# Performance work log

Hardware: AMD Instinct MI355X
Metric: run time of the kernel (lower is better)

## Reference

```python
import jax, jax.numpy as jnp
import numpy as np

DEPTH = 3

def _rx(theta):
    c, s = jnp.cos(theta / 2), jnp.sin(theta / 2)
    return jnp.stack([jnp.stack([c + 0j, -1j * s], -1),
                      jnp.stack([-1j * s, c + 0j], -1)], -2)

def _ry(theta):
    c, s = jnp.cos(theta / 2), jnp.sin(theta / 2)
    return jnp.stack([jnp.stack([c + 0j, -s + 0j], -1),
                      jnp.stack([s + 0j, c + 0j], -1)], -2)

def _rz(theta):
    e = jnp.exp(-0.5j * theta.astype(jnp.complex64))
    z = jnp.zeros_like(e)
    return jnp.stack([jnp.stack([e, z], -1),
                      jnp.stack([z, jnp.conj(e)], -1)], -2)

def _apply_1q(state, U, q):
    # state: (batch, 2,2,...,2); wire q lives on axis q+1. U: (2,2) or (batch,2,2)
    s = jnp.moveaxis(state, q + 1, -1)
    if U.ndim == 3:
        s = jnp.einsum('b...i,bji->b...j', s, U)
    else:
        s = jnp.einsum('...i,ji->...j', s, U)
    return jnp.moveaxis(s, -1, q + 1)

def _apply_cnot(state, c, t):
    s = jnp.moveaxis(state, (c + 1, t + 1), (-2, -1))
    s = jnp.concatenate([s[..., 0:1, :], s[..., 1:2, ::-1]], axis=-2)
    return jnp.moveaxis(s, (-2, -1), (c + 1, t + 1))

def _circuit(x, params):
    batch, n = x.shape
    depth = params.shape[0]
    state = jnp.zeros((batch,) + (2,) * n, jnp.complex64)
    state = state.at[(slice(None),) + (0,) * n].set(1.0)
    # data-encoding RX with per-sample angles
    for q in range(n):
        state = _apply_1q(state, _rx(x[:, q].astype(jnp.complex64).real), q)
    for l in range(depth):
        for q in range(n):
            state = _apply_1q(state, _rx(params[l, q, 0]), q)
            state = _apply_1q(state, _ry(params[l, q, 1]), q)
            state = _apply_1q(state, _rz(params[l, q, 2]), q)
        for q in range(n - 1):
            state = _apply_cnot(state, q, q + 1)
        state = _apply_cnot(state, n - 1, 0)
    probs = state.real ** 2 + state.imag ** 2  # (batch, 2,...,2)
    exps = []
    for w in range(n):
        p = jnp.moveaxis(probs, w + 1, 1).reshape(batch, 2, -1).sum(-1)
        exps.append(p[:, 0] - p[:, 1])  # <Z_w> = P(0) - P(1)
    return jnp.stack(exps, axis=1)


def setup_inputs() -> dict:
    key = jax.random.key(0)
    k1, k2 = jax.random.split(key)
    batch, n = 128, 14
    x = jax.random.normal(k1, (batch, n), dtype=jnp.float32)
    params = jax.random.normal(k2, (DEPTH, n, 3), dtype=jnp.float32)
    return {"x": x, "params": params}


def reference(x, params):
    return _circuit(x, params)
```

## Files before the change

### kernel.cpp

```cpp
#include <hip/hip_runtime.h>

namespace {

using v2f = __attribute__((ext_vector_type(2))) float;

constexpr int NQ      = 14;
constexpr int NSTATES = 1 << NQ;
constexpr int BLOCK   = 1024;
constexpr int NWAVES  = BLOCK / 64;

constexpr unsigned cparity(unsigned x){ x^=x>>8; x^=x>>4; x^=x>>2; x^=x>>1; return x&1u; }

struct Mat { unsigned row[NQ]; unsigned col[NQ]; };

constexpr Mat m_after(int nr){
  Mat m{};
  for(int p=0;p<NQ;++p){ m.row[p]=1u<<p; m.col[p]=1u<<p; }
  for(int l=0;l<nr;++l)
    for(int q=0;q<NQ;++q){
      int cq=(q==NQ-1)?NQ-1:q, tq=(q==NQ-1)?0:q+1;
      int Pc=NQ-1-cq, Pt=NQ-1-tq;
      m.row[Pt]^=m.row[Pc]; m.col[Pc]^=m.col[Pt];
    }
  return m;
}

constexpr Mat M1=m_after(1), M2=m_after(2), M3=m_after(3);
constexpr unsigned amask(int q){ return M1.col[NQ-1-q]; }
constexpr unsigned arow (int q){ return M1.row[NQ-1-q]; }
constexpr unsigned bmask(int q){ return M2.col[NQ-1-q]; }
constexpr unsigned brow (int q){ return M2.row[NQ-1-q]; }

constexpr int rank_of(const unsigned* v, int n){
  unsigned a[24]{};
  for(int i=0;i<n;++i) a[i]=v[i];
  int r=0;
  for(int bit=15;bit>=0;--bit){
    int p=-1;
    for(int i=r;i<n;++i){ if((a[i]>>bit)&1){ p=i; break; } }
    if(p<0) continue;
    unsigned t=a[r]; a[r]=a[p]; a[p]=t;
    for(int i=0;i<n;++i) if(i!=r && ((a[i]>>bit)&1)) a[i]^=a[r];
    ++r;
  }
  return r;
}

struct Plan {
  unsigned A[14], B[14], C[14];
  int BlaneGi[6]; unsigned BlanePi4[6];
  int BregGi[4];  unsigned BregEps[4];
  int CregGi[4];  unsigned CregEps[4];
  int ClaneGi[4]; unsigned ClaneEps[4];
  unsigned EJ4[14], ET[14];
};

constexpr Plan make_plan(){
  Plan P{};
  for(int t=0;t<14;++t) P.A[t]=amask(t);
  for(int t=0;t<4;++t){ P.B[t]=amask(10+t); P.BregGi[t]=10+t; }
  bool used[14]{}; int picked[14]{}; int np=0;
  {
    unsigned cur[20]{}; int nc=0;
    for(int t=0;t<4;++t) cur[nc++]=P.B[t];
    for(int q=0;q<14 && np<10;++q){
      cur[nc]=bmask(q);
      if(rank_of(cur,nc+1)==nc+1){ ++nc; picked[np++]=q; used[q]=true; }
    }
  }
  for(int i=0;i<6;++i){ P.B[4+i]=bmask(picked[i]); P.BlaneGi[i]=14+picked[i]; }
  int wq[4]{}, un[4]{}; int nu=0;
  for(int i=0;i<4;++i){ wq[i]=picked[6+i]; P.B[10+i]=bmask(wq[i]); P.CregGi[i]=14+wq[i]; }
  for(int q=0;q<14;++q) if(!used[q]) un[nu++]=q;
  for(int i=0;i<4;++i) P.ClaneGi[i]=14+un[i];
  for(int i=0;i<4;++i){ unsigned m=0;
    for(int t=0;t<10;++t) m |= cparity(arow(10+i)&P.B[4+t])<<t;
    P.BregEps[i]=m; }
  for(int i=0;i<6;++i){ unsigned m=0;
    for(int t=0;t<4;++t) m |= cparity(brow(picked[i])&P.B[t])<<t;
    P.BlanePi4[i]=m; }
  for(int t=0;t<4;++t) P.C[t]=bmask(wq[t]);
  for(int t=0;t<4;++t) P.C[4+t]=bmask(un[t]);
  {
    unsigned cc[20]{}; int n=0;
    for(int t=0;t<8;++t) cc[n++]=P.C[t];
    int pos=8;
    for(int p=0;p<14 && pos<14;++p){
      cc[n]=1u<<p;
      if(rank_of(cc,n+1)==n+1){ P.C[pos]=1u<<p; ++n; ++pos; }
    }
  }
  for(int i=0;i<4;++i){ unsigned m=0;
    for(int t=0;t<10;++t) m |= cparity(brow(wq[i])&P.C[4+t])<<t;
    P.CregEps[i]=m; }
  for(int i=0;i<4;++i){ unsigned m=0;
    for(int t=0;t<10;++t){ if(t==i) continue; m |= cparity(brow(un[i])&P.C[4+t])<<t; }
    P.ClaneEps[i]=m; }
  for(int w=0;w<14;++w){
    unsigned R=M3.row[NQ-1-w]; unsigned mj=0, mt=0;
    for(int t=0;t<4;++t)  mj |= cparity(R&P.C[t])<<t;
    for(int t=0;t<10;++t) mt |= cparity(R&P.C[4+t])<<t;
    P.EJ4[w]=mj; P.ET[w]=mt;
  }
  return P;
}

constexpr Plan PL = make_plan();
static_assert(rank_of(PL.A,14)==14, "phase A map not bijective");
static_assert(rank_of(PL.B,14)==14, "phase B map not bijective");
static_assert(rank_of(PL.C,14)==14, "phase C map not bijective");

struct Inv { unsigned col[NQ]; };
constexpr Inv inv_basis(const unsigned* bas){
  unsigned vec[NQ]{}, cmb[NQ]{}; bool used[NQ]{}; int pivk[NQ]{};
  for(int k=0;k<NQ;++k){ vec[k]=bas[k]; cmb[k]=1u<<k; }
  for(int b=0;b<NQ;++b){
    int p=-1;
    for(int k=0;k<NQ;++k) if(!used[k] && ((vec[k]>>b)&1)){ p=k; break; }
    used[p]=true; pivk[b]=p;
    for(int k=0;k<NQ;++k) if(k!=p && ((vec[k]>>b)&1)){ vec[k]^=vec[p]; cmb[k]^=cmb[p]; }
  }
  Inv R{};
  for(int b=0;b<NQ;++b) R.col[b]=cmb[pivk[b]];
  return R;
}
constexpr bool check_inv(const unsigned* bas, const Inv& iv){
  for(int p=0;p<NQ;++p){
    unsigned s=0;
    for(int k=0;k<NQ;++k) if((iv.col[p]>>k)&1) s^=bas[k];
    if(s != (1u<<p)) return false;
  }
  return true;
}
constexpr Inv IA = inv_basis(PL.A), IB = inv_basis(PL.B), IC = inv_basis(PL.C);
static_assert(check_inv(PL.A, IA), "IA");
static_assert(check_inv(PL.B, IB), "IB");
static_assert(check_inv(PL.C, IC), "IC");

struct Trans { unsigned t[NQ]; };
constexpr Trans trans_phys(const Inv& iv){
  Trans T{};
  for(int p=0;p<NQ;++p) T.t[p]=iv.col[p];
  return T;
}
constexpr Trans trans_of(const unsigned* cur, const Inv& iv){
  Trans T{};
  for(int k=0;k<NQ;++k){
    unsigned c=0;
    for(int p=0;p<NQ;++p) if((cur[k]>>p)&1) c^=iv.col[p];
    T.t[k]=c;
  }
  return T;
}
constexpr Trans T_PA = trans_phys(IA);
constexpr Trans T_AB = trans_of(PL.A, IB);
constexpr Trans T_BC = trans_of(PL.B, IC);

struct CJ { unsigned v[16]; };
constexpr CJ mk_cj(const Trans& T){
  CJ c{};
  for(int j=0;j<16;++j){
    unsigned s=0;
    for(int b=0;b<4;++b) if((j>>b)&1) s^=T.t[b];
    c.v[j]=s;
  }
  return c;
}
constexpr CJ CJ_PA=mk_cj(T_PA), CJ_AB=mk_cj(T_AB), CJ_BC=mk_cj(T_BC);

__device__ __forceinline__ v2f mkv(float a, float b){ v2f r; r[0]=a; r[1]=b; return r; }

__device__ __forceinline__ v2f pk_mul(v2f a, v2f b){
  v2f d; asm("v_pk_mul_f32 %0, %1, %2 op_sel:[0,0] op_sel_hi:[1,1]" : "=v"(d) : "v"(a), "v"(b)); return d;
}
__device__ __forceinline__ v2f pk_fma(v2f a, v2f b, v2f c){
  v2f d; asm("v_pk_fma_f32 %0, %1, %2, %3 op_sel:[0,0,0] op_sel_hi:[1,1,1]" : "=v"(d) : "v"(a), "v"(b), "v"(c)); return d;
}
__device__ __forceinline__ v2f pk_fma_swap1(v2f a, v2f b, v2f c){
  v2f d; asm("v_pk_fma_f32 %0, %1, %2, %3 op_sel:[0,1,0] op_sel_hi:[1,0,1]" : "=v"(d) : "v"(a), "v"(b), "v"(c)); return d;
}
__device__ __forceinline__ v2f cmul_pk(v2f uxx, v2f uyn, v2f s){ return pk_fma_swap1(uyn, s, pk_mul(uxx, s)); }
__device__ __forceinline__ v2f cfma_pk(v2f uxx, v2f uyn, v2f s, v2f acc){ return pk_fma_swap1(uyn, s, pk_fma(uxx, s, acc)); }

__device__ __forceinline__ float2 cmulf(float2 a, float2 b){
  return make_float2(a.x*b.x - a.y*b.y, a.x*b.y + a.y*b.x);
}
__device__ __forceinline__ v2f sel2(bool c, v2f x, v2f y){ v2f r; r[0]=c?x[0]:y[0]; r[1]=c?x[1]:y[1]; return r; }

struct GC { v2f u00x,u00n,u01x,u01n,u10x,u10n,u11x,u11n; };
__device__ __forceinline__ GC load_gc(const v2f* __restrict__ g){
  GC c{g[0],g[1],g[2],g[3],g[4],g[5],g[6],g[7]}; return c;
}

template<int CTRL>
__device__ __forceinline__ int dpp(int x){
  return __builtin_amdgcn_update_dpp(0, x, CTRL, 0xF, 0xF, true);
}
__device__ __forceinline__ int x32(int x, unsigned lane){
  auto r = __builtin_amdgcn_permlane32_swap((unsigned)x, (unsigned)x, false, false);
  return (lane & 32u) ? (int)r[0] : (int)r[1];
}
template<int K>
__device__ __forceinline__ v2f xpart(v2f v, unsigned lane){
  int x0=__float_as_int(v[0]), x1=__float_as_int(v[1]);
  int y0, y1;
  if constexpr (K==0){ y0=dpp<0xB1>(x0);  y1=dpp<0xB1>(x1); }
  else if constexpr (K==1){ y0=dpp<0x4E>(x0);  y1=dpp<0x4E>(x1); }
  else if constexpr (K==2){
    y0=__builtin_amdgcn_ds_swizzle(x0,0x101F);
    y1=__builtin_amdgcn_ds_swizzle(x1,0x101F);
  }
  else if constexpr (K==3){ y0=dpp<0x128>(x0); y1=dpp<0x128>(x1); }
  else if constexpr (K==4){
    y0=__builtin_amdgcn_ds_swizzle(x0,0x401F);
    y1=__builtin_amdgcn_ds_swizzle(x1,0x401F);
  }
  else { y0=x32(x0,lane); y1=x32(x1,lane); }
  v2f r; r[0]=__int_as_float(y0); r[1]=__int_as_float(y1); return r;
}

template<int BIT>
__device__ __forceinline__ void reg_gate(v2f (&a)[16], const GC& c, bool eps){
  v2f m00x=sel2(eps,c.u11x,c.u00x), m00n=sel2(eps,c.u11n,c.u00n);
  v2f m01x=sel2(eps,c.u10x,c.u01x), m01n=sel2(eps,c.u10n,c.u01n);
  v2f m10x=sel2(eps,c.u01x,c.u10x), m10n=sel2(eps,c.u01n,c.u10n);
  v2f m11x=sel2(eps,c.u00x,c.u11x), m11n=sel2(eps,c.u00n,c.u11n);
#pragma unroll
  for(int v=0; v<16; ++v){
    if(!((v>>BIT)&1)){
      int w = v | (1<<BIT);
      v2f a0=a[v], a1=a[w];
      a[v] = cfma_pk(m01x,m01n,a1, cmul_pk(m00x,m00n,a0));
      a[w] = cfma_pk(m11x,m11n,a1, cmul_pk(m10x,m10n,a0));
    }
  }
}

template<int XK, unsigned PI4>
__device__ __forceinline__ void lane_gate(v2f (&a)[16], const GC& c, bool sel, unsigned lane){
  v2f kax0=sel2(sel,c.u11x,c.u00x), kan0=sel2(sel,c.u11n,c.u00n);
  v2f kbx0=sel2(sel,c.u10x,c.u01x), kbn0=sel2(sel,c.u10n,c.u01n);
  v2f kax1=sel2(sel,c.u00x,c.u11x), kan1=sel2(sel,c.u00n,c.u11n);
  v2f kbx1=sel2(sel,c.u01x,c.u10x), kbn1=sel2(sel,c.u01n,c.u10n);
#pragma unroll
  for(int h=0;h<2;++h){
    v2f th[8];
#pragma unroll
    for(int jj=0;jj<8;++jj) th[jj] = xpart<XK>(a[h*8+jj], lane);
#pragma unroll
    for(int jj=0;jj<8;++jj){
      const int j = h*8+jj;
      constexpr unsigned PP = PI4;
      bool pi = (__builtin_popcount(PP & (unsigned)j) & 1) != 0;
      v2f kax = pi?kax1:kax0, kan = pi?kan1:kan0;
      v2f kbx = pi?kbx1:kbx0, kbn = pi?kbn1:kbn0;
      a[j] = cfma_pk(kbx,kbn,th[jj], cmul_pk(kax,kan,a[j]));
    }
  }
}

__device__ __forceinline__ unsigned nb_of(unsigned tid, const unsigned (&t)[NQ]){
  unsigned s=0;
#pragma unroll
  for(int k=0;k<10;++k) s ^= t[4+k] & (0u-((tid>>k)&1u));
  return s;
}

__device__ __forceinline__ void scatter16(v2f* __restrict__ st, const v2f (&a)[16],
                                          unsigned nb, const CJ& cj){
#pragma unroll
  for(int j=0;j<16;++j){
    unsigned d = nb ^ cj.v[j];
    st[d + (d>>4)] = a[j];
  }
}

__global__ __launch_bounds__(BLOCK, 4) void qsim_kernel(
    const float* __restrict__ x,
    const float* __restrict__ prm,
    float* __restrict__ out)
{
  __shared__ v2f    st[BLOCK*17];
  __shared__ v2f    Utab[28*8];
  __shared__ float2 l0c[NQ][2];
  __shared__ float  red[NWAVES][NQ];

  const int b = blockIdx.x;
  const unsigned tid = threadIdx.x;
  const unsigned lane = tid & 63u;

  if(tid < 28){
    int t = tid;
    int l = 1 + t/NQ, q = t % NQ;
    float ax=prm[(l*NQ+q)*3+0], ay=prm[(l*NQ+q)*3+1], az=prm[(l*NQ+q)*3+2];
    float cx,sx,cy,sy,cz,sz;
    sincosf(0.5f*ax,&sx,&cx); sincosf(0.5f*ay,&sy,&cy); sincosf(0.5f*az,&sz,&cz);
    float2 M00=make_float2(cy*cx, sy*sx),  M01=make_float2(-sy*cx,-cy*sx);
    float2 M10=make_float2(sy*cx,-cy*sx),  M11=make_float2(cy*cx,-sy*sx);
    float2 ez =make_float2(cz,-sz), ezc=make_float2(cz,sz);
    float2 U00=cmulf(ez,M00), U01=cmulf(ez,M01), U10=cmulf(ezc,M10), U11=cmulf(ezc,M11);
    v2f* U = &Utab[t*8];
    U[0]=mkv(U00.x,U00.x); U[1]=mkv(-U00.y,U00.y);
    U[2]=mkv(U01.x,U01.x); U[3]=mkv(-U01.y,U01.y);
    U[4]=mkv(U10.x,U10.x); U[5]=mkv(-U10.y,U10.y);
    U[6]=mkv(U11.x,U11.x); U[7]=mkv(-U11.y,U11.y);
  }
  if(tid < NQ){
    int q = tid;
    float ax = prm[q*3+0] + x[b*NQ+q];
    float ay = prm[q*3+1], az = prm[q*3+2];
    float cx,sx,cy,sy,cz,sz;
    sincosf(0.5f*ax,&sx,&cx); sincosf(0.5f*ay,&sy,&cy); sincosf(0.5f*az,&sz,&cz);
    l0c[q][0] = cmulf(make_float2(cz,-sz), make_float2(cy*cx,  sy*sx));
    l0c[q][1] = cmulf(make_float2(cz, sz), make_float2(sy*cx, -cy*sx));
  }
  __syncthreads();

  {
    float2 Pk = l0c[0][(tid>>9)&1];
#pragma unroll
    for(int q=1;q<10;++q) Pk = cmulf(Pk, l0c[q][(tid>>(9-q))&1]);
    float2 t2[2], t4[4];
    t2[0]=cmulf(Pk,l0c[10][0]); t2[1]=cmulf(Pk,l0c[10][1]);
#pragma unroll
    for(int i=0;i<2;++i){ t4[2*i]=cmulf(t2[i],l0c[11][0]); t4[2*i+1]=cmulf(t2[i],l0c[11][1]); }
    v2f a[16];
#pragma unroll
    for(int j=0;j<16;++j){
      float2 v = cmulf(cmulf(t4[j>>2], l0c[12][(j>>1)&1]), l0c[13][j&1]);
      a[j] = mkv(v.x, v.y);
    }
    scatter16(st, a, nb_of(tid, T_PA.t), CJ_PA);
  }
  __syncthreads();

  {
    v2f a[16];
    const int rb = (int)tid*17;
#pragma unroll
    for(int j=0;j<16;++j) a[j] = st[rb + j];
    reg_gate<0>(a, load_gc(Utab+0*8), false);
    reg_gate<1>(a, load_gc(Utab+1*8), false);
    reg_gate<2>(a, load_gc(Utab+2*8), false);
    reg_gate<3>(a, load_gc(Utab+3*8), false);
    lane_gate<0,0u>(a, load_gc(Utab+4*8), (tid&1)!=0,  lane);
    lane_gate<1,0u>(a, load_gc(Utab+5*8), (tid&2)!=0,  lane);
    lane_gate<2,0u>(a, load_gc(Utab+6*8), (tid&4)!=0,  lane);
    lane_gate<3,0u>(a, load_gc(Utab+7*8), (tid&8)!=0,  lane);
    lane_gate<4,0u>(a, load_gc(Utab+8*8), (tid&16)!=0, lane);
    lane_gate<5,0u>(a, load_gc(Utab+9*8), (tid&32)!=0, lane);
    __syncthreads();
    scatter16(st, a, nb_of(tid, T_AB.t), CJ_AB);
  }
  __syncthreads();

  {
    v2f a[16];
    const int rb = (int)tid*17;
#pragma unroll
    for(int j=0;j<16;++j) a[j] = st[rb + j];
    reg_gate<0>(a, load_gc(Utab+PL.BregGi[0]*8), (__builtin_popcount(PL.BregEps[0]&tid)&1)!=0);
    reg_gate<1>(a, load_gc(Utab+PL.BregGi[1]*8), (__builtin_popcount(PL.BregEps[1]&tid)&1)!=0);
    reg_gate<2>(a, load_gc(Utab+PL.BregGi[2]*8), (__builtin_popcount(PL.BregEps[2]&tid)&1)!=0);
    reg_gate<3>(a, load_gc(Utab+PL.BregGi[3]*8), (__builtin_popcount(PL.BregEps[3]&tid)&1)!=0);
    lane_gate<0,PL.BlanePi4[0]>(a, load_gc(Utab+PL.BlaneGi[0]*8), (tid&1)!=0,  lane);
    lane_gate<1,PL.BlanePi4[1]>(a, load_gc(Utab+PL.BlaneGi[1]*8), (tid&2)!=0,  lane);
    lane_gate<2,PL.BlanePi4[2]>(a, load_gc(Utab+PL.BlaneGi[2]*8), (tid&4)!=0,  lane);
    lane_gate<3,PL.BlanePi4[3]>(a, load_gc(Utab+PL.BlaneGi[3]*8), (tid&8)!=0,  lane);
    lane_gate<4,PL.BlanePi4[4]>(a, load_gc(Utab+PL.BlaneGi[4]*8), (tid&16)!=0, lane);
    lane_gate<5,PL.BlanePi4[5]>(a, load_gc(Utab+PL.BlaneGi[5]*8), (tid&32)!=0, lane);
    __syncthreads();
    scatter16(st, a, nb_of(tid, T_BC.t), CJ_BC);
  }
  __syncthreads();

  {
    v2f a[16];
    const int rb = (int)tid*17;
#pragma unroll
    for(int j=0;j<16;++j) a[j] = st[rb + j];
    reg_gate<0>(a, load_gc(Utab+PL.CregGi[0]*8), (__builtin_popcount(PL.CregEps[0]&tid)&1)!=0);
    reg_gate<1>(a, load_gc(Utab+PL.CregGi[1]*8), (__builtin_popcount(PL.CregEps[1]&tid)&1)!=0);
    reg_gate<2>(a, load_gc(Utab+PL.CregGi[2]*8), (__builtin_popcount(PL.CregEps[2]&tid)&1)!=0);
    reg_gate<3>(a, load_gc(Utab+PL.CregGi[3]*8), (__builtin_popcount(PL.CregEps[3]&tid)&1)!=0);
    lane_gate<0,0u>(a, load_gc(Utab+PL.ClaneGi[0]*8),
        (((tid&1u)!=0) != ((__builtin_popcount(PL.ClaneEps[0]&tid)&1)!=0)), lane);
    lane_gate<1,0u>(a, load_gc(Utab+PL.ClaneGi[1]*8),
        (((tid&2u)!=0) != ((__builtin_popcount(PL.ClaneEps[1]&tid)&1)!=0)), lane);
    lane_gate<2,0u>(a, load_gc(Utab+PL.ClaneGi[2]*8),
        (((tid&4u)!=0) != ((__builtin_popcount(PL.ClaneEps[2]&tid)&1)!=0)), lane);
    lane_gate<3,0u>(a, load_gc(Utab+PL.ClaneGi[3]*8),
        (((tid&8u)!=0) != ((__builtin_popcount(PL.ClaneEps[3]&tid)&1)!=0)), lane);

    float acc[NQ];
#pragma unroll
    for(int w=0;w<NQ;++w) acc[w]=0.f;
#pragma unroll
    for(int j=0;j<16;++j){
      float p = a[j][0]*a[j][0] + a[j][1]*a[j][1];
#pragma unroll
      for(int w=0;w<NQ;++w){
        if(__builtin_popcount(PL.EJ4[w] & (unsigned)j) & 1) acc[w]-=p; else acc[w]+=p;
      }
    }
    const int wave = tid >> 6;
#pragma unroll
    for(int w=0;w<NQ;++w){
      float v = (__builtin_popcount(PL.ET[w]&tid)&1) ? -acc[w] : acc[w];
#pragma unroll
      for(int off=32; off>0; off>>=1) v += __shfl_down(v, off, 64);
      if(lane==0) red[wave][w]=v;
    }
    __syncthreads();
    if(tid < NQ){
      float s=0.f;
#pragma unroll
      for(int wv=0; wv<NWAVES; ++wv) s += red[wv][tid];
      out[b*NQ + tid] = s;
    }
  }
}

}

extern "C" void kernel_launch(void* const* d_in, const int* in_sizes, int n_in,
                              void* d_out, int out_size, void* d_ws, size_t ws_size,
                              hipStream_t stream) {
  const float* x   = (const float*)d_in[0];
  const float* prm = (const float*)d_in[1];
  float* out = (float*)d_out;
  const int batch = in_sizes[0] / NQ;
  qsim_kernel<<<batch, BLOCK, 0, stream>>>(x, prm, out);
}
```

Measured before the change: 39.63 us.

## Split single-block simulation into three phase kernels through global workspace

```diff
diff --git a/kernel.cpp b/kernel.cpp
--- a/kernel.cpp
+++ b/kernel.cpp
@@ -4,10 +4,10 @@
 
 using v2f = __attribute__((ext_vector_type(2))) float;
 
-constexpr int NQ      = 14;
-constexpr int NSTATES = 1 << NQ;
-constexpr int BLOCK   = 1024;
-constexpr int NWAVES  = BLOCK / 64;
+constexpr int NQ     = 14;
+constexpr int NST    = 1 << NQ;
+constexpr int BLOCK  = 512;
+constexpr int NWAVES = BLOCK / 64;
 
 constexpr unsigned cparity(unsigned x){ x^=x>>8; x^=x>>4; x^=x>>2; x^=x>>1; return x&1u; }
 
@@ -46,127 +46,84 @@
   return r;
 }
 
-struct Plan {
-  unsigned A[14], B[14], C[14];
-  int BlaneGi[6]; unsigned BlanePi4[6];
-  int BregGi[4];  unsigned BregEps[4];
-  int CregGi[4];  unsigned CregEps[4];
-  int ClaneGi[4]; unsigned ClaneEps[4];
-  unsigned EJ4[14], ET[14];
+struct Sel {
+  int picked[6], wq[4], un[4];
+  unsigned Gen[3][10];
+  unsigned Row[3][10];
+  unsigned BlanePi4[6];
+  unsigned EJ4[NQ];
+  int lq[3][10][2];
 };
 
-constexpr Plan make_plan(){
-  Plan P{};
-  for(int t=0;t<14;++t) P.A[t]=amask(t);
-  for(int t=0;t<4;++t){ P.B[t]=amask(10+t); P.BregGi[t]=10+t; }
+constexpr Sel make_sel(){
+  Sel S{};
+  unsigned cur[24]{}; int nc=0;
+  for(int t=0;t<4;++t) cur[nc++]=amask(10+t);
   bool used[14]{}; int picked[14]{}; int np=0;
-  {
-    unsigned cur[20]{}; int nc=0;
-    for(int t=0;t<4;++t) cur[nc++]=P.B[t];
-    for(int q=0;q<14 && np<10;++q){
-      cur[nc]=bmask(q);
-      if(rank_of(cur,nc+1)==nc+1){ ++nc; picked[np++]=q; used[q]=true; }
-    }
-  }
-  for(int i=0;i<6;++i){ P.B[4+i]=bmask(picked[i]); P.BlaneGi[i]=14+picked[i]; }
-  int wq[4]{}, un[4]{}; int nu=0;
-  for(int i=0;i<4;++i){ wq[i]=picked[6+i]; P.B[10+i]=bmask(wq[i]); P.CregGi[i]=14+wq[i]; }
-  for(int q=0;q<14;++q) if(!used[q]) un[nu++]=q;
-  for(int i=0;i<4;++i) P.ClaneGi[i]=14+un[i];
-  for(int i=0;i<4;++i){ unsigned m=0;
-    for(int t=0;t<10;++t) m |= cparity(arow(10+i)&P.B[4+t])<<t;
-    P.BregEps[i]=m; }
+  for(int q=0;q<14 && np<10;++q){
+    cur[nc]=bmask(q);
+    if(rank_of(cur,nc+1)==nc+1){ ++nc; picked[np++]=q; used[q]=true; }
+  }
+  for(int i=0;i<6;++i) S.picked[i]=picked[i];
+  for(int i=0;i<4;++i) S.wq[i]=picked[6+i];
+  { int nu=0; for(int q=0;q<14;++q) if(!used[q]) S.un[nu++]=q; }
   for(int i=0;i<6;++i){ unsigned m=0;
-    for(int t=0;t<4;++t) m |= cparity(brow(picked[i])&P.B[t])<<t;
-    P.BlanePi4[i]=m; }
-  for(int t=0;t<4;++t) P.C[t]=bmask(wq[t]);
-  for(int t=0;t<4;++t) P.C[4+t]=bmask(un[t]);
-  {
-    unsigned cc[20]{}; int n=0;
-    for(int t=0;t<8;++t) cc[n++]=P.C[t];
+    for(int t=0;t<4;++t) m |= cparity(brow(picked[i]) & amask(10+t))<<t;
+    S.BlanePi4[i]=m; }
+  for(int g=0;g<10;++g){ S.Gen[0][g]=amask(g);    S.Row[0][g]=arow(g);    S.lq[0][g][0]=1; S.lq[0][g][1]=g; }
+  for(int g=0;g<4;++g) { S.Gen[1][g]=amask(10+g); S.Row[1][g]=arow(10+g); S.lq[1][g][0]=1; S.lq[1][g][1]=10+g; }
+  for(int g=0;g<6;++g) { S.Gen[1][4+g]=bmask(picked[g]); S.Row[1][4+g]=brow(picked[g]);
+                         S.lq[1][4+g][0]=2; S.lq[1][4+g][1]=picked[g]; }
+  for(int g=0;g<4;++g) { S.Gen[2][g]=bmask(S.wq[g]); S.Row[2][g]=brow(S.wq[g]);
+                         S.lq[2][g][0]=2; S.lq[2][g][1]=S.wq[g]; }
+  for(int g=0;g<4;++g) { S.Gen[2][4+g]=bmask(S.un[g]); S.Row[2][4+g]=brow(S.un[g]);
+                         S.lq[2][4+g][0]=2; S.lq[2][4+g][1]=S.un[g]; }
+  { unsigned cc[24]{}; int n=0;
+    for(int t=0;t<8;++t) cc[n++]=S.Gen[2][t];
     int pos=8;
-    for(int p=0;p<14 && pos<14;++p){
+    for(int p=0;p<14 && pos<10;++p){
       cc[n]=1u<<p;
-      if(rank_of(cc,n+1)==n+1){ P.C[pos]=1u<<p; ++n; ++pos; }
-    }
-  }
-  for(int i=0;i<4;++i){ unsigned m=0;
-    for(int t=0;t<10;++t) m |= cparity(brow(wq[i])&P.C[4+t])<<t;
-    P.CregEps[i]=m; }
-  for(int i=0;i<4;++i){ unsigned m=0;
-    for(int t=0;t<10;++t){ if(t==i) continue; m |= cparity(brow(un[i])&P.C[4+t])<<t; }
-    P.ClaneEps[i]=m; }
-  for(int w=0;w<14;++w){
-    unsigned R=M3.row[NQ-1-w]; unsigned mj=0, mt=0;
-    for(int t=0;t<4;++t)  mj |= cparity(R&P.C[t])<<t;
-    for(int t=0;t<10;++t) mt |= cparity(R&P.C[4+t])<<t;
-    P.EJ4[w]=mj; P.ET[w]=mt;
-  }
-  return P;
-}
-
-constexpr Plan PL = make_plan();
-static_assert(rank_of(PL.A,14)==14, "phase A map not bijective");
-static_assert(rank_of(PL.B,14)==14, "phase B map not bijective");
-static_assert(rank_of(PL.C,14)==14, "phase C map not bijective");
-
-struct Inv { unsigned col[NQ]; };
-constexpr Inv inv_basis(const unsigned* bas){
-  unsigned vec[NQ]{}, cmb[NQ]{}; bool used[NQ]{}; int pivk[NQ]{};
-  for(int k=0;k<NQ;++k){ vec[k]=bas[k]; cmb[k]=1u<<k; }
-  for(int b=0;b<NQ;++b){
+      if(rank_of(cc,n+1)==n+1){ S.Gen[2][pos]=1u<<p; S.Row[2][pos]=0; ++n; ++pos; }
+    } }
+  for(int w=0;w<NQ;++w){
+    unsigned R=M3.row[NQ-1-w]; unsigned mj=0;
+    for(int t=0;t<4;++t) mj |= cparity(R & S.Gen[2][t])<<t;
+    S.EJ4[w]=mj;
+  }
+  return S;
+}
+constexpr Sel SL = make_sel();
+static_assert(rank_of(SL.Gen[0],10)==10, "K0 gens");
+static_assert(rank_of(SL.Gen[1],10)==10, "K1 gens");
+static_assert(rank_of(SL.Gen[2],10)==10, "K2 gens");
+
+struct Ins { unsigned ins[10]; };
+constexpr Ins make_ins(const unsigned* gen){
+  unsigned a[10]{}; for(int i=0;i<10;++i) a[i]=gen[i];
+  int piv[10]{}; int r=0;
+  for(int bit=13;bit>=0;--bit){
     int p=-1;
-    for(int k=0;k<NQ;++k) if(!used[k] && ((vec[k]>>b)&1)){ p=k; break; }
-    used[p]=true; pivk[b]=p;
-    for(int k=0;k<NQ;++k) if(k!=p && ((vec[k]>>b)&1)){ vec[k]^=vec[p]; cmb[k]^=cmb[p]; }
-  }
-  Inv R{};
-  for(int b=0;b<NQ;++b) R.col[b]=cmb[pivk[b]];
-  return R;
-}
-constexpr bool check_inv(const unsigned* bas, const Inv& iv){
-  for(int p=0;p<NQ;++p){
-    unsigned s=0;
-    for(int k=0;k<NQ;++k) if((iv.col[p]>>k)&1) s^=bas[k];
-    if(s != (1u<<p)) return false;
-  }
-  return true;
-}
-constexpr Inv IA = inv_basis(PL.A), IB = inv_basis(PL.B), IC = inv_basis(PL.C);
-static_assert(check_inv(PL.A, IA), "IA");
-static_assert(check_inv(PL.B, IB), "IB");
-static_assert(check_inv(PL.C, IC), "IC");
-
-struct Trans { unsigned t[NQ]; };
-constexpr Trans trans_phys(const Inv& iv){
-  Trans T{};
-  for(int p=0;p<NQ;++p) T.t[p]=iv.col[p];
-  return T;
-}
-constexpr Trans trans_of(const unsigned* cur, const Inv& iv){
-  Trans T{};
-  for(int k=0;k<NQ;++k){
-    unsigned c=0;
-    for(int p=0;p<NQ;++p) if((cur[k]>>p)&1) c^=iv.col[p];
-    T.t[k]=c;
-  }
-  return T;
-}
-constexpr Trans T_PA = trans_phys(IA);
-constexpr Trans T_AB = trans_of(PL.A, IB);
-constexpr Trans T_BC = trans_of(PL.B, IC);
-
-struct CJ { unsigned v[16]; };
-constexpr CJ mk_cj(const Trans& T){
-  CJ c{};
-  for(int j=0;j<16;++j){
-    unsigned s=0;
-    for(int b=0;b<4;++b) if((j>>b)&1) s^=T.t[b];
-    c.v[j]=s;
-  }
+    for(int i=r;i<10;++i){ if((a[i]>>bit)&1){ p=i; break; } }
+    if(p<0) continue;
+    unsigned t=a[r]; a[r]=a[p]; a[p]=t;
+    for(int i=0;i<10;++i) if(i!=r && ((a[i]>>bit)&1)) a[i]^=a[r];
+    piv[r++]=bit;
+  }
+  for(int i=0;i<10;++i) for(int j=i+1;j<10;++j)
+    if(piv[j]<piv[i]){ int t=piv[i]; piv[i]=piv[j]; piv[j]=t; }
+  Ins I{};
+  for(int g=0;g<10;++g) I.ins[g]=(1u<<piv[g])-1u;
+  return I;
+}
+constexpr Ins INS0=make_ins(SL.Gen[0]), INS1=make_ins(SL.Gen[1]), INS2=make_ins(SL.Gen[2]);
+
+struct CJ16 { unsigned v[16]; };
+constexpr CJ16 make_cj(const unsigned* gen){
+  CJ16 c{};
+  for(int j=0;j<16;++j){ unsigned s=0; for(int b=0;b<4;++b) if((j>>b)&1) s^=gen[b]; c.v[j]=s; }
   return c;
 }
-constexpr CJ CJ_PA=mk_cj(T_PA), CJ_AB=mk_cj(T_AB), CJ_BC=mk_cj(T_BC);
+constexpr CJ16 CJ0=make_cj(SL.Gen[0]), CJ1=make_cj(SL.Gen[1]), CJ2=make_cj(SL.Gen[2]);
 
 __device__ __forceinline__ v2f mkv(float a, float b){ v2f r; r[0]=a; r[1]=b; return r; }
 
@@ -250,8 +207,7 @@
 #pragma unroll
     for(int jj=0;jj<8;++jj){
       const int j = h*8+jj;
-      constexpr unsigned PP = PI4;
-      bool pi = (__builtin_popcount(PP & (unsigned)j) & 1) != 0;
+      bool pi = (__builtin_popcount(PI4 & (unsigned)j) & 1) != 0;
       v2f kax = pi?kax1:kax0, kan = pi?kan1:kan0;
       v2f kbx = pi?kbx1:kbx0, kbn = pi?kbn1:kbn0;
       a[j] = cfma_pk(kbx,kbn,th[jj], cmul_pk(kax,kan,a[j]));
@@ -259,39 +215,24 @@
   }
 }
 
-__device__ __forceinline__ unsigned nb_of(unsigned tid, const unsigned (&t)[NQ]){
-  unsigned s=0;
-#pragma unroll
-  for(int k=0;k<10;++k) s ^= t[4+k] & (0u-((tid>>k)&1u));
-  return s;
-}
-
-__device__ __forceinline__ void scatter16(v2f* __restrict__ st, const v2f (&a)[16],
-                                          unsigned nb, const CJ& cj){
-#pragma unroll
-  for(int j=0;j<16;++j){
-    unsigned d = nb ^ cj.v[j];
-    st[d + (d>>4)] = a[j];
-  }
-}
-
-__global__ __launch_bounds__(BLOCK, 4) void qsim_kernel(
-    const float* __restrict__ x,
-    const float* __restrict__ prm,
-    float* __restrict__ out)
+template<int PH>
+__global__ __launch_bounds__(BLOCK, 2) void qk(
+    const float* __restrict__ x, const float* __restrict__ prm,
+    v2f* __restrict__ ws, float* __restrict__ out, int batch)
 {
-  __shared__ v2f    st[BLOCK*17];
-  __shared__ v2f    Utab[28*8];
+  __shared__ v2f    Utab[10*8];
   __shared__ float2 l0c[NQ][2];
   __shared__ float  red[NWAVES][NQ];
 
-  const int b = blockIdx.x;
+  const int bid = blockIdx.x;
+  const int piece = (bid >= batch) ? 1 : 0;
+  const int s = bid - piece*batch;
   const unsigned tid = threadIdx.x;
   const unsigned lane = tid & 63u;
 
-  if(tid < 28){
-    int t = tid;
-    int l = 1 + t/NQ, q = t % NQ;
+  constexpr int NG = (PH==2) ? 8 : 10;
+  if(tid < NG){
+    int l = SL.lq[PH][tid][0], q = SL.lq[PH][tid][1];
     float ax=prm[(l*NQ+q)*3+0], ay=prm[(l*NQ+q)*3+1], az=prm[(l*NQ+q)*3+2];
     float cx,sx,cy,sy,cz,sz;
     sincosf(0.5f*ax,&sx,&cx); sincosf(0.5f*ay,&sy,&cy); sincosf(0.5f*az,&sz,&cz);
@@ -299,99 +240,80 @@
     float2 M10=make_float2(sy*cx,-cy*sx),  M11=make_float2(cy*cx,-sy*sx);
     float2 ez =make_float2(cz,-sz), ezc=make_float2(cz,sz);
     float2 U00=cmulf(ez,M00), U01=cmulf(ez,M01), U10=cmulf(ezc,M10), U11=cmulf(ezc,M11);
-    v2f* U = &Utab[t*8];
+    v2f* U = &Utab[tid*8];
     U[0]=mkv(U00.x,U00.x); U[1]=mkv(-U00.y,U00.y);
     U[2]=mkv(U01.x,U01.x); U[3]=mkv(-U01.y,U01.y);
     U[4]=mkv(U10.x,U10.x); U[5]=mkv(-U10.y,U10.y);
     U[6]=mkv(U11.x,U11.x); U[7]=mkv(-U11.y,U11.y);
   }
-  if(tid < NQ){
-    int q = tid;
-    float ax = prm[q*3+0] + x[b*NQ+q];
-    float ay = prm[q*3+1], az = prm[q*3+2];
-    float cx,sx,cy,sy,cz,sz;
-    sincosf(0.5f*ax,&sx,&cx); sincosf(0.5f*ay,&sy,&cy); sincosf(0.5f*az,&sz,&cz);
-    l0c[q][0] = cmulf(make_float2(cz,-sz), make_float2(cy*cx,  sy*sx));
-    l0c[q][1] = cmulf(make_float2(cz, sz), make_float2(sy*cx, -cy*sx));
+  if constexpr (PH==0){
+    if(tid < NQ){
+      int q = tid;
+      float ax = prm[q*3+0] + x[s*NQ+q];
+      float ay = prm[q*3+1], az = prm[q*3+2];
+      float cx,sx,cy,sy,cz,sz;
+      sincosf(0.5f*ax,&sx,&cx); sincosf(0.5f*ay,&sy,&cy); sincosf(0.5f*az,&sz,&cz);
+      l0c[q][0] = cmulf(make_float2(cz,-sz), make_float2(cy*cx,  sy*sx));
+      l0c[q][1] = cmulf(make_float2(cz, sz), make_float2(sy*cx, -cy*sx));
+    }
   }
   __syncthreads();
 
-  {
-    float2 Pk = l0c[0][(tid>>9)&1];
-#pragma unroll
-    for(int q=1;q<10;++q) Pk = cmulf(Pk, l0c[q][(tid>>(9-q))&1]);
-    float2 t2[2], t4[4];
-    t2[0]=cmulf(Pk,l0c[10][0]); t2[1]=cmulf(Pk,l0c[10][1]);
-#pragma unroll
-    for(int i=0;i<2;++i){ t4[2*i]=cmulf(t2[i],l0c[11][0]); t4[2*i+1]=cmulf(t2[i],l0c[11][1]); }
-    v2f a[16];
+  constexpr Ins  INS = (PH==0)?INS0:(PH==1)?INS1:INS2;
+  constexpr CJ16 CJ  = (PH==0)?CJ0:(PH==1)?CJ1:CJ2;
+  unsigned e = (tid>>6) | ((unsigned)piece<<3);
+#pragma unroll
+  for(int g=0; g<10; ++g) e = ((e & ~INS.ins[g])<<1) | (e & INS.ins[g]);
+  unsigned s0t = e;
+#pragma unroll
+  for(int k=0;k<6;++k) s0t ^= SL.Gen[PH][4+k] & (0u - ((tid>>k)&1u));
+
+  v2f* __restrict__ base = ws + (size_t)s*NST;
+
+  v2f a[16];
+  if constexpr (PH==0){
 #pragma unroll
     for(int j=0;j<16;++j){
-      float2 v = cmulf(cmulf(t4[j>>2], l0c[12][(j>>1)&1]), l0c[13][j&1]);
-      a[j] = mkv(v.x, v.y);
-    }
-    scatter16(st, a, nb_of(tid, T_PA.t), CJ_PA);
-  }
-  __syncthreads();
-
-  {
-    v2f a[16];
-    const int rb = (int)tid*17;
-#pragma unroll
-    for(int j=0;j<16;++j) a[j] = st[rb + j];
-    reg_gate<0>(a, load_gc(Utab+0*8), false);
-    reg_gate<1>(a, load_gc(Utab+1*8), false);
-    reg_gate<2>(a, load_gc(Utab+2*8), false);
-    reg_gate<3>(a, load_gc(Utab+3*8), false);
-    lane_gate<0,0u>(a, load_gc(Utab+4*8), (tid&1)!=0,  lane);
-    lane_gate<1,0u>(a, load_gc(Utab+5*8), (tid&2)!=0,  lane);
-    lane_gate<2,0u>(a, load_gc(Utab+6*8), (tid&4)!=0,  lane);
-    lane_gate<3,0u>(a, load_gc(Utab+7*8), (tid&8)!=0,  lane);
-    lane_gate<4,0u>(a, load_gc(Utab+8*8), (tid&16)!=0, lane);
-    lane_gate<5,0u>(a, load_gc(Utab+9*8), (tid&32)!=0, lane);
-    __syncthreads();
-    scatter16(st, a, nb_of(tid, T_AB.t), CJ_AB);
-  }
-  __syncthreads();
-
-  {
-    v2f a[16];
-    const int rb = (int)tid*17;
-#pragma unroll
-    for(int j=0;j<16;++j) a[j] = st[rb + j];
-    reg_gate<0>(a, load_gc(Utab+PL.BregGi[0]*8), (__builtin_popcount(PL.BregEps[0]&tid)&1)!=0);
-    reg_gate<1>(a, load_gc(Utab+PL.BregGi[1]*8), (__builtin_popcount(PL.BregEps[1]&tid)&1)!=0);
-    reg_gate<2>(a, load_gc(Utab+PL.BregGi[2]*8), (__builtin_popcount(PL.BregEps[2]&tid)&1)!=0);
-    reg_gate<3>(a, load_gc(Utab+PL.BregGi[3]*8), (__builtin_popcount(PL.BregEps[3]&tid)&1)!=0);
-    lane_gate<0,PL.BlanePi4[0]>(a, load_gc(Utab+PL.BlaneGi[0]*8), (tid&1)!=0,  lane);
-    lane_gate<1,PL.BlanePi4[1]>(a, load_gc(Utab+PL.BlaneGi[1]*8), (tid&2)!=0,  lane);
-    lane_gate<2,PL.BlanePi4[2]>(a, load_gc(Utab+PL.BlaneGi[2]*8), (tid&4)!=0,  lane);
-    lane_gate<3,PL.BlanePi4[3]>(a, load_gc(Utab+PL.BlaneGi[3]*8), (tid&8)!=0,  lane);
-    lane_gate<4,PL.BlanePi4[4]>(a, load_gc(Utab+PL.BlaneGi[4]*8), (tid&16)!=0, lane);
-    lane_gate<5,PL.BlanePi4[5]>(a, load_gc(Utab+PL.BlaneGi[5]*8), (tid&32)!=0, lane);
-    __syncthreads();
-    scatter16(st, a, nb_of(tid, T_BC.t), CJ_BC);
-  }
-  __syncthreads();
-
-  {
-    v2f a[16];
-    const int rb = (int)tid*17;
-#pragma unroll
-    for(int j=0;j<16;++j) a[j] = st[rb + j];
-    reg_gate<0>(a, load_gc(Utab+PL.CregGi[0]*8), (__builtin_popcount(PL.CregEps[0]&tid)&1)!=0);
-    reg_gate<1>(a, load_gc(Utab+PL.CregGi[1]*8), (__builtin_popcount(PL.CregEps[1]&tid)&1)!=0);
-    reg_gate<2>(a, load_gc(Utab+PL.CregGi[2]*8), (__builtin_popcount(PL.CregEps[2]&tid)&1)!=0);
-    reg_gate<3>(a, load_gc(Utab+PL.CregGi[3]*8), (__builtin_popcount(PL.CregEps[3]&tid)&1)!=0);
-    lane_gate<0,0u>(a, load_gc(Utab+PL.ClaneGi[0]*8),
-        (((tid&1u)!=0) != ((__builtin_popcount(PL.ClaneEps[0]&tid)&1)!=0)), lane);
-    lane_gate<1,0u>(a, load_gc(Utab+PL.ClaneGi[1]*8),
-        (((tid&2u)!=0) != ((__builtin_popcount(PL.ClaneEps[1]&tid)&1)!=0)), lane);
-    lane_gate<2,0u>(a, load_gc(Utab+PL.ClaneGi[2]*8),
-        (((tid&4u)!=0) != ((__builtin_popcount(PL.ClaneEps[2]&tid)&1)!=0)), lane);
-    lane_gate<3,0u>(a, load_gc(Utab+PL.ClaneGi[3]*8),
-        (((tid&8u)!=0) != ((__builtin_popcount(PL.ClaneEps[3]&tid)&1)!=0)), lane);
-
+      unsigned p = s0t ^ CJ.v[j];
+      float2 acc = l0c[0][(p>>13)&1];
+#pragma unroll
+      for(int q=1;q<NQ;++q) acc = cmulf(acc, l0c[q][(p>>(13-q))&1]);
+      a[j] = mkv(acc.x, acc.y);
+    }
+  } else {
+#pragma unroll
+    for(int j=0;j<16;++j) a[j] = base[s0t ^ CJ.v[j]];
+  }
+
+  reg_gate<0>(a, load_gc(Utab+0*8), (__builtin_popcount(SL.Row[PH][0]&s0t)&1)!=0);
+  reg_gate<1>(a, load_gc(Utab+1*8), (__builtin_popcount(SL.Row[PH][1]&s0t)&1)!=0);
+  reg_gate<2>(a, load_gc(Utab+2*8), (__builtin_popcount(SL.Row[PH][2]&s0t)&1)!=0);
+  reg_gate<3>(a, load_gc(Utab+3*8), (__builtin_popcount(SL.Row[PH][3]&s0t)&1)!=0);
+  if constexpr (PH==0){
+    lane_gate<0,0u>(a, load_gc(Utab+4*8), (__builtin_popcount(SL.Row[0][4]&s0t)&1)!=0, lane);
+    lane_gate<1,0u>(a, load_gc(Utab+5*8), (__builtin_popcount(SL.Row[0][5]&s0t)&1)!=0, lane);
+    lane_gate<2,0u>(a, load_gc(Utab+6*8), (__builtin_popcount(SL.Row[0][6]&s0t)&1)!=0, lane);
+    lane_gate<3,0u>(a, load_gc(Utab+7*8), (__builtin_popcount(SL.Row[0][7]&s0t)&1)!=0, lane);
+    lane_gate<4,0u>(a, load_gc(Utab+8*8), (__builtin_popcount(SL.Row[0][8]&s0t)&1)!=0, lane);
+    lane_gate<5,0u>(a, load_gc(Utab+9*8), (__builtin_popcount(SL.Row[0][9]&s0t)&1)!=0, lane);
+  } else if constexpr (PH==1){
+    lane_gate<0,SL.BlanePi4[0]>(a, load_gc(Utab+4*8), (__builtin_popcount(SL.Row[1][4]&s0t)&1)!=0, lane);
+    lane_gate<1,SL.BlanePi4[1]>(a, load_gc(Utab+5*8), (__builtin_popcount(SL.Row[1][5]&s0t)&1)!=0, lane);
+    lane_gate<2,SL.BlanePi4[2]>(a, load_gc(Utab+6*8), (__builtin_popcount(SL.Row[1][6]&s0t)&1)!=0, lane);
+    lane_gate<3,SL.BlanePi4[3]>(a, load_gc(Utab+7*8), (__builtin_popcount(SL.Row[1][7]&s0t)&1)!=0, lane);
+    lane_gate<4,SL.BlanePi4[4]>(a, load_gc(Utab+8*8), (__builtin_popcount(SL.Row[1][8]&s0t)&1)!=0, lane);
+    lane_gate<5,SL.BlanePi4[5]>(a, load_gc(Utab+9*8), (__builtin_popcount(SL.Row[1][9]&s0t)&1)!=0, lane);
+  } else {
+    lane_gate<0,0u>(a, load_gc(Utab+4*8), (__builtin_popcount(SL.Row[2][4]&s0t)&1)!=0, lane);
+    lane_gate<1,0u>(a, load_gc(Utab+5*8), (__builtin_popcount(SL.Row[2][5]&s0t)&1)!=0, lane);
+    lane_gate<2,0u>(a, load_gc(Utab+6*8), (__builtin_popcount(SL.Row[2][6]&s0t)&1)!=0, lane);
+    lane_gate<3,0u>(a, load_gc(Utab+7*8), (__builtin_popcount(SL.Row[2][7]&s0t)&1)!=0, lane);
+  }
+
+  if constexpr (PH<2){
+#pragma unroll
+    for(int j=0;j<16;++j) base[s0t ^ CJ.v[j]] = a[j];
+  } else {
     float acc[NQ];
 #pragma unroll
     for(int w=0;w<NQ;++w) acc[w]=0.f;
@@ -400,23 +322,23 @@
       float p = a[j][0]*a[j][0] + a[j][1]*a[j][1];
 #pragma unroll
       for(int w=0;w<NQ;++w){
-        if(__builtin_popcount(PL.EJ4[w] & (unsigned)j) & 1) acc[w]-=p; else acc[w]+=p;
+        if(__builtin_popcount(SL.EJ4[w] & (unsigned)j) & 1) acc[w]-=p; else acc[w]+=p;
       }
     }
     const int wave = tid >> 6;
 #pragma unroll
     for(int w=0;w<NQ;++w){
-      float v = (__builtin_popcount(PL.ET[w]&tid)&1) ? -acc[w] : acc[w];
+      float v = (__builtin_popcount(M3.row[NQ-1-w] & s0t)&1) ? -acc[w] : acc[w];
 #pragma unroll
       for(int off=32; off>0; off>>=1) v += __shfl_down(v, off, 64);
       if(lane==0) red[wave][w]=v;
     }
     __syncthreads();
     if(tid < NQ){
-      float s=0.f;
-#pragma unroll
-      for(int wv=0; wv<NWAVES; ++wv) s += red[wv][tid];
-      out[b*NQ + tid] = s;
+      float t=0.f;
+#pragma unroll
+      for(int wv=0; wv<NWAVES; ++wv) t += red[wv][tid];
+      atomicAdd(&out[s*NQ + tid], t);
     }
   }
 }
@@ -430,5 +352,10 @@
   const float* prm = (const float*)d_in[1];
   float* out = (float*)d_out;
   const int batch = in_sizes[0] / NQ;
-  qsim_kernel<<<batch, BLOCK, 0, stream>>>(x, prm, out);
-}
+  v2f* ws = (v2f*)d_ws;
+
+  hipMemsetAsync(d_out, 0, (size_t)out_size*sizeof(float), stream);
+  qk<0><<<2*batch, BLOCK, 0, stream>>>(x, prm, ws, out, batch);
+  qk<1><<<2*batch, BLOCK, 0, stream>>>(x, prm, ws, out, batch);
+  qk<2><<<2*batch, BLOCK, 0, stream>>>(x, prm, ws, out, batch);
+}
```

Measured after the change: 55.10 us. 39.0% more time.
